# Optimization experiments

Hardware: AMD Instinct MI355X
Metric: run time of the kernel (lower is better)

The kernel has to match this reference:

```python
import jax, jax.numpy as jnp
import numpy as np

B, S, E, H, FF = 4, 2048, 512, 8, 2048
DH = E // H
EPS = 1e-6


def setup_inputs() -> dict:
    key = jax.random.key(0)
    ks = jax.random.split(key, 16)
    sc = lambda fan_in: 1.0 / np.sqrt(fan_in)
    inp = {
        "x": jax.random.normal(ks[0], (B, S, E), dtype=jnp.float32),
        "src_mask": jnp.ones((B, 1, 1, S), dtype=jnp.int32),
        # attention projections, stored [in, out]
        "wq": jax.random.uniform(ks[1], (E, E), minval=-sc(E), maxval=sc(E)),
        "bq": jnp.zeros((E,), jnp.float32),
        "wk": jax.random.uniform(ks[2], (E, E), minval=-sc(E), maxval=sc(E)),
        "bk": jnp.zeros((E,), jnp.float32),
        "wv": jax.random.uniform(ks[3], (E, E), minval=-sc(E), maxval=sc(E)),
        "bv": jnp.zeros((E,), jnp.float32),
        "wo": jax.random.uniform(ks[4], (E, E), minval=-sc(E), maxval=sc(E)),
        "bo": jnp.zeros((E,), jnp.float32),
        # feed-forward
        "w1": jax.random.uniform(ks[5], (E, FF), minval=-sc(E), maxval=sc(E)),
        "b1": jnp.zeros((FF,), jnp.float32),
        "w2": jax.random.uniform(ks[6], (FF, E), minval=-sc(FF), maxval=sc(FF)),
        "b2": jnp.zeros((E,), jnp.float32),
        # addNormLayer scalar params (alpha init 1, bias init 0)
        "alpha1": jnp.ones((1,), jnp.float32),
        "beta1": jnp.zeros((1,), jnp.float32),
        "alpha2": jnp.ones((1,), jnp.float32),
        "beta2": jnp.zeros((1,), jnp.float32),
    }
    return inp


def _norm(x, alpha, beta):
    # matches torch: mean + unbiased std (ddof=1), eps added to std
    mean = jnp.mean(x, axis=-1, keepdims=True)
    std = jnp.std(x, axis=-1, keepdims=True, ddof=1)
    return alpha * (x - mean) / (std + EPS) + beta


def reference(x, src_mask, wq, bq, wk, bk, wv, bv, wo, bo,
              w1, b1, w2, b2, alpha1, beta1, alpha2, beta2):
    # --- residual 1: pre-norm self-attention ---
    n = _norm(x, alpha1, beta1)  # [B,S,E]
    q = (n @ wq + bq).reshape(B, S, H, DH).transpose(0, 2, 1, 3)  # [B,H,S,DH]
    k = (n @ wk + bk).reshape(B, S, H, DH).transpose(0, 2, 1, 3)
    v = (n @ wv + bv).reshape(B, S, H, DH).transpose(0, 2, 1, 3)
    scores = jnp.einsum('bhqd,bhkd->bhqk', q, k) / np.sqrt(DH)  # [B,H,S,S]
    scores = jnp.where(src_mask == 0, -1e9, scores)
    attn = jax.nn.softmax(scores, axis=-1)
    ctx = jnp.einsum('bhqk,bhkd->bhqd', attn, v)  # [B,H,S,DH]
    ctx = ctx.transpose(0, 2, 1, 3).reshape(B, S, E)
    x = x + (ctx @ wo + bo)
    # --- residual 2: pre-norm FFN ---
    n2 = _norm(x, alpha2, beta2)
    ff = jax.nn.relu(n2 @ w1 + b1) @ w2 + b2
    return x + ff
```

## Files before the change

kernel.cpp:

```cpp
#include <hip/hip_runtime.h>
#include <type_traits>

typedef __bf16 bfrag __attribute__((ext_vector_type(8)));
typedef float f32x4 __attribute__((ext_vector_type(4)));
typedef float f32x16 __attribute__((ext_vector_type(16)));
typedef unsigned short us8 __attribute__((ext_vector_type(8)));
typedef unsigned int u32x2 __attribute__((ext_vector_type(2)));
typedef unsigned int u32x4 __attribute__((ext_vector_type(4)));

__device__ __forceinline__ float bf2f(unsigned short s) {
  unsigned u = ((unsigned)s) << 16;
  float f;
  __builtin_memcpy(&f, &u, 4);
  return f;
}
__device__ __forceinline__ unsigned short f2bf(float f) {
  unsigned u;
  __builtin_memcpy(&u, &f, 4);
  u += 0x7fffu + ((u >> 16) & 1u);
  return (unsigned short)(u >> 16);
}
__device__ __forceinline__ float rdf(const void* p, size_t i, int isf) {
  return isf ? ((const float*)p)[i] : bf2f(((const unsigned short*)p)[i]);
}
__device__ __forceinline__ void gld16(const unsigned short* g, unsigned short* l) {
  __builtin_amdgcn_global_load_lds(
      (const __attribute__((address_space(1))) unsigned int*)g,
      (__attribute__((address_space(3))) unsigned int*)l, 16, 0, 0);
}
__device__ __forceinline__ unsigned cvtpk_bf16(float a, float b) {
  unsigned d;
  asm("v_cvt_pk_bf16_f32 %0, %1, %2" : "=v"(d) : "v"(a), "v"(b));
  return d;
}

template <int XMODE>
__device__ void norm_unit(const void* xin, const void* alpha, const void* beta,
                          unsigned short* out, int isf, int u) {
  constexpr int E = 512;
  int xf = XMODE ? 1 : isf;
  int tid = threadIdx.x;
  int wave = tid >> 6, lane = tid & 63;
  size_t tok = (size_t)u * 4 + wave;
  float v[8];
  if (xf) {
    const float* xp = (const float*)xin + tok * E + lane * 8;
    float4 a0 = *(const float4*)xp;
    float4 a1 = *(const float4*)(xp + 4);
    v[0] = a0.x; v[1] = a0.y; v[2] = a0.z; v[3] = a0.w;
    v[4] = a1.x; v[5] = a1.y; v[6] = a1.z; v[7] = a1.w;
  } else {
    us8 uu = *(const us8*)((const unsigned short*)xin + tok * E + lane * 8);
#pragma unroll
    for (int j = 0; j < 8; j++) v[j] = bf2f(uu[j]);
  }
  float s = 0.f, sq = 0.f;
#pragma unroll
  for (int j = 0; j < 8; j++) { s += v[j]; sq += v[j] * v[j]; }
#pragma unroll
  for (int off = 1; off < 64; off <<= 1) {
    s += __shfl_xor(s, off, 64);
    sq += __shfl_xor(sq, off, 64);
  }
  float mean = s * (1.0f / 512.0f);
  float var = fmaxf((sq - 512.0f * mean * mean) * (1.0f / 511.0f), 0.0f);
  float inv = rdf(alpha, 0, isf) / (sqrtf(var) + 1e-6f);
  float be = rdf(beta, 0, isf);
  us8 ov;
#pragma unroll
  for (int j = 0; j < 8; j++) ov[j] = f2bf((v[j] - mean) * inv + be);
  *(us8*)(out + tok * E + lane * 8) = ov;
}

__global__ __launch_bounds__(256) void setup_k(
    const unsigned short* __restrict__ x16,
    const void* wq, const void* wk, const void* wv, const void* wo,
    const void* w1, const void* w2,
    unsigned short* wqkvT, unsigned short* woT,
    unsigned short* w1T, unsigned short* w2T,
    const void* bq, const void* bk, const void* bv, const void* bo,
    const void* b1, const void* b2, float* __restrict__ bcat,
    const void* alpha1, const void* beta1, unsigned short* __restrict__ n1,
    int* __restrict__ flag) {
  __shared__ unsigned short tile[32][33];
  __shared__ int s_cnt;
  int tid = threadIdx.x;
  int bid = blockIdx.x;
  if (tid == 0) s_cnt = 0;
  __syncthreads();
  {
    int c = 0;
    for (int i = tid; i < 4096; i += 256) {
      unsigned short s = x16[2 * i];
      int e = (s >> 7) & 0xFF;
      if (e > 0xC2 || (e != 0 && e < 0x3D)) c++;
    }
    atomicAdd(&s_cnt, c);
  }
  __syncthreads();
  const int isf = (s_cnt > 256) ? 1 : 0;
  if (bid == 0 && tid == 0) flag[0] = isf;

  if (bid >= 3090) {
    norm_unit<0>(x16, alpha1, beta1, n1, isf, bid - 3090);
    return;
  }
  if (bid >= 3072) {
    int i = (bid - 3072) * 256 + tid;
    if (i < 4608) {
      float v;
      if (i < 512) v = rdf(bq, i, isf);
      else if (i < 1024) v = rdf(bk, i - 512, isf);
      else if (i < 1536) v = rdf(bv, i - 1024, isf);
      else if (i < 2048) v = rdf(bo, i - 1536, isf);
      else if (i < 4096) v = rdf(b1, i - 2048, isf);
      else v = rdf(b2, i - 4096, isf);
      bcat[i] = v;
    }
    return;
  }
  const void* W;
  unsigned short* Wt;
  int K, N, t;
  if (bid < 1024) {
    K = 512; N = 512; t = bid & 255;
    if (bid < 256) { W = wq; Wt = wqkvT; }
    else if (bid < 512) { W = wk; Wt = wqkvT + 262144; }
    else if (bid < 768) { W = wv; Wt = wqkvT + 524288; }
    else { W = wo; Wt = woT; }
  } else if (bid < 2048) {
    W = w1; Wt = w1T; K = 512; N = 2048; t = bid - 1024;
  } else {
    W = w2; Wt = w2T; K = 2048; N = 512; t = bid - 2048;
  }
  int nx = N >> 5;
  int n0 = (t % nx) * 32, k0 = (t / nx) * 32;
#pragma unroll
  for (int i = 0; i < 4; i++) {
    int e = tid + i * 256;
    int r = e >> 5, c = e & 31;
    tile[r][c] = f2bf(rdf(W, (size_t)(k0 + r) * N + n0 + c, isf));
  }
  __syncthreads();
#pragma unroll
  for (int i = 0; i < 4; i++) {
    int e = tid + i * 256;
    int r = e >> 5, c = e & 31;
    Wt[(size_t)(n0 + r) * K + k0 + c] = tile[c][r];
  }
}

__global__ __launch_bounds__(256) void vtrans_k(
    const unsigned short* __restrict__ qkb, unsigned short* __restrict__ vbt) {
  __shared__ unsigned short tile[32][33];
  int tid = threadIdx.x;
  int u = blockIdx.x;
  int s0 = (u & 63) * 32;
  int d0 = ((u >> 6) & 1) * 32;
  int bh = u >> 7, b = bh >> 3, h = bh & 7;
#pragma unroll
  for (int i = 0; i < 4; i++) {
    int e = tid + i * 256;
    int r = e >> 5, c = e & 31;
    tile[r][c] = qkb[((size_t)b * 2048 + s0 + r) * 1536 + 1024 + h * 64 + d0 + c];
  }
  __syncthreads();
#pragma unroll
  for (int i = 0; i < 4; i++) {
    int e = tid + i * 256;
    int r = e >> 5, c = e & 31;
    vbt[((size_t)bh * 64 + d0 + r) * 2048 + s0 + c] = tile[c][r];
  }
}

__global__ __launch_bounds__(256) void norm2_k(
    const void* __restrict__ xin, const void* __restrict__ alpha,
    const void* __restrict__ beta, unsigned short* __restrict__ out,
    const int* __restrict__ flag) {
  norm_unit<1>(xin, alpha, beta, out, flag[0], blockIdx.x);
}

template <int TN, int RES, int OUTM, int RELU>
__global__ __launch_bounds__(256, 3) void gemm2_k(
    const unsigned short* __restrict__ A,
    const unsigned short* __restrict__ Bt,
    const float* __restrict__ bias,
    const void* __restrict__ res,
    void* __restrict__ outp,
    int N, int K, const int* __restrict__ flag) {
  constexpr int MT = (TN == 128) ? 4 : 2;
  constexpr int BROWS = TN / 4;
  __shared__ alignas(16) unsigned short As[128 * 64];
  __shared__ alignas(16) unsigned short Bs[TN * 64];
  int isf = flag[0];
  int outf32 = (OUTM == 1) || (OUTM == 2 && isf);
  int tid = threadIdx.x;
  int wave = tid >> 6, lane = tid & 63;
  int quad = lane >> 4, l16 = lane & 15, l7 = l16 & 7;
  int wm = (TN == 128) ? (wave >> 1) : wave;
  int wn = (TN == 128) ? (wave & 1) : 0;
  size_t m0 = (size_t)blockIdx.x * 128;
  size_t n0 = (size_t)blockIdx.y * TN;

  int lrow = lane >> 3;
  int gcol = 8 * ((lane & 7) ^ lrow);

  const unsigned short* ag = A + (m0 + wave * 32 + lrow) * K + gcol;
  const unsigned short* bg = Bt + (n0 + wave * BROWS + lrow) * K + gcol;
  unsigned short* asl = &As[(wave * 32) * 64];
  unsigned short* bsl = &Bs[(wave * BROWS) * 64];

  f32x4 acc[MT][4];
#pragma unroll
  for (int i = 0; i < MT; i++)
#pragma unroll
    for (int j = 0; j < 4; j++) acc[i][j] = {0.f, 0.f, 0.f, 0.f};

  for (int k0 = 0; k0 < K; k0 += 64) {
    __syncthreads();
#pragma unroll
    for (int c = 0; c < 4; c++)
      gld16(ag + (size_t)(8 * c) * K + k0, asl + (8 * c) * 64);
#pragma unroll
    for (int c = 0; c < BROWS / 8; c++)
      gld16(bg + (size_t)(8 * c) * K + k0, bsl + (8 * c) * 64);
    __syncthreads();
#pragma unroll
    for (int ko = 0; ko < 2; ko++) {
      int slot = ((4 * ko + quad) ^ l7) * 8;
      bfrag af[MT], bf[4];
#pragma unroll
      for (int i = 0; i < MT; i++)
        af[i] = *(const bfrag*)&As[(wm * (MT * 16) + i * 16 + l16) * 64 + slot];
#pragma unroll
      for (int j = 0; j < 4; j++)
        bf[j] = *(const bfrag*)&Bs[(wn * 64 + j * 16 + l16) * 64 + slot];
#pragma unroll
      for (int i = 0; i < MT; i++)
#pragma unroll
        for (int j = 0; j < 4; j++)
          acc[i][j] = __builtin_amdgcn_mfma_f32_16x16x32_bf16(af[i], bf[j], acc[i][j], 0, 0, 0);
    }
  }
#pragma unroll
  for (int j = 0; j < 4; j++) {
    size_t n = n0 + wn * 64 + j * 16 + l16;
    float bv = bias[n];
#pragma unroll
    for (int i = 0; i < MT; i++) {
#pragma unroll
      for (int r = 0; r < 4; r++) {
        size_t m = m0 + wm * (MT * 16) + i * 16 + quad * 4 + r;
        float vv = acc[i][j][r] + bv;
        if (RELU) vv = fmaxf(vv, 0.0f);
        if (RES == 1) vv += rdf(res, m * N + n, isf);
        else if (RES == 2) vv += ((const float*)res)[m * N + n];
        if (outf32) ((float*)outp)[m * N + n] = vv;
        else ((unsigned short*)outp)[m * N + n] = f2bf(vv);
      }
    }
  }
}

__global__ __launch_bounds__(512, 4) void attn_k(
    const unsigned short* __restrict__ qkb,
    const unsigned short* __restrict__ vbt,
    const int* __restrict__ mask,
    unsigned short* __restrict__ ctx) {
  constexpr int S = 2048;
  __shared__ alignas(16) unsigned short Kt[2][2][64 * 64];
  __shared__ alignas(16) unsigned short Vt[2][2][64 * 64];
  __shared__ alignas(16) float mskf[S];
  __shared__ float ml[2][128];
  __shared__ int s_all;
  int tid = threadIdx.x, wave = tid >> 6, lane = tid & 63;
  int kh = wave >> 2, wv = wave & 3;
  int l32 = lane & 31, hi = lane >> 5;

  int lin = blockIdx.x;
  int work = (lin & 7) * 64 + (lin >> 3);
  int bh = work >> 4;
  int q0 = (work & 15) * 128;
  int b = bh >> 3, h = bh & 7;
  size_t rowbase = (size_t)b * S;
  const float SC = 0.18033688f;

  bfrag qf[4];
  {
    const unsigned short* qp =
        qkb + (rowbase + q0 + wv * 32 + l32) * 1536 + h * 64 + hi * 8;
#pragma unroll
    for (int ds = 0; ds < 4; ds++) qf[ds] = *(const bfrag*)(qp + ds * 16);
  }

  int srow_l = lane >> 3;
  int sc = lane & 7;
  int swz = (sc ^ srow_l) * 8;
  const unsigned short* kgb = qkb + 512 + h * 64;
  const unsigned short* vgb = vbt + (size_t)bh * 64 * S;

  const unsigned short* kp[2];
  const unsigned short* vp[2];
#pragma unroll
  for (int i = 0; i < 2; i++) {
    int r = wv * 16 + i * 8 + srow_l;
    kp[i] = kgb + (rowbase + kh * 1024 + r) * 1536 + swz;
    vp[i] = vgb + (size_t)r * S + kh * 1024 + swz;
  }

  auto STAGE = [&](int buf) {
#pragma unroll
    for (int i = 0; i < 2; i++) {
      gld16(kp[i], &Kt[kh][buf][(wv * 16 + i * 8) * 64]);
      kp[i] += 64 * 1536;
      gld16(vp[i], &Vt[kh][buf][(wv * 16 + i * 8) * 64]);
      vp[i] += 64;
    }
  };

  f32x16 o[2];
#pragma unroll
  for (int i = 0; i < 16; i++) { o[0][i] = 0.f; o[1][i] = 0.f; }
  f32x16 z16;
#pragma unroll
  for (int i = 0; i < 16; i++) z16[i] = 0.f;
  float l_i = 0.f;

  STAGE(0);
  if (tid == 0) s_all = 1;
  __syncthreads();
  {
    int ok = 1;
    for (int i = tid; i < S; i += 512) {
      int mv = mask[rowbase + i];
      ok &= (mv != 0);
      mskf[i] = mv ? 0.0f : -1e5f;
    }
    atomicAnd(&s_all, ok);
  }
  __syncthreads();
  int am = s_all;

  auto BODY = [&](auto amc) {
    constexpr bool AM = decltype(amc)::value;
    for (int it = 0; it < 16; it++) {
      int cur = it & 1;
      if (it + 1 < 16) STAGE(cur ^ 1);

      f32x16 pacc[2];
#pragma unroll
      for (int t = 0; t < 2; t++) {
        int r = t * 32 + l32;
#pragma unroll
        for (int ds = 0; ds < 4; ds++) {
          int phys = ((2 * ds + hi) ^ (l32 & 7)) * 8;
          bfrag kf = *(const bfrag*)&Kt[kh][cur][r * 64 + phys];
          pacc[t] = __builtin_amdgcn_mfma_f32_32x32x16_bf16(
              kf, qf[ds], ds == 0 ? z16 : pacc[t], 0, 0, 0);
        }
      }

      unsigned pb[16];
#pragma unroll
      for (int t = 0; t < 2; t++) {
#pragma unroll
        for (int g = 0; g < 4; g++) {
          float p0, p1, p2, p3;
          if constexpr (AM) {
            p0 = __builtin_amdgcn_exp2f(pacc[t][g * 4 + 0] * SC);
            p1 = __builtin_amdgcn_exp2f(pacc[t][g * 4 + 1] * SC);
            p2 = __builtin_amdgcn_exp2f(pacc[t][g * 4 + 2] * SC);
            p3 = __builtin_amdgcn_exp2f(pacc[t][g * 4 + 3] * SC);
          } else {
            float4 m4 =
                *(const float4*)&mskf[kh * 1024 + it * 64 + t * 32 + g * 8 + hi * 4];
            p0 = __builtin_amdgcn_exp2f(fmaf(pacc[t][g * 4 + 0], SC, m4.x));
            p1 = __builtin_amdgcn_exp2f(fmaf(pacc[t][g * 4 + 1], SC, m4.y));
            p2 = __builtin_amdgcn_exp2f(fmaf(pacc[t][g * 4 + 2], SC, m4.z));
            p3 = __builtin_amdgcn_exp2f(fmaf(pacc[t][g * 4 + 3], SC, m4.w));
          }
          l_i += (p0 + p1) + (p2 + p3);
          pb[t * 8 + g * 2] = cvtpk_bf16(p0, p1);
          pb[t * 8 + g * 2 + 1] = cvtpk_bf16(p2, p3);
        }
      }

#pragma unroll
      for (int ks = 0; ks < 4; ks++) {
        int t = ks >> 1, e = ks & 1;
        u32x2 sA = __builtin_amdgcn_permlane32_swap(
            pb[t * 8 + 4 * e + 0], pb[t * 8 + 4 * e + 2], false, false);
        u32x2 sB = __builtin_amdgcn_permlane32_swap(
            pb[t * 8 + 4 * e + 1], pb[t * 8 + 4 * e + 3], false, false);
        u32x4 pw = {sA.x, sB.x, sA.y, sB.y};
        bfrag pf = __builtin_bit_cast(bfrag, pw);
#pragma unroll
        for (int dt = 0; dt < 2; dt++) {
          int r = dt * 32 + l32;
          int phys = ((2 * ks + hi) ^ (l32 & 7)) * 8;
          bfrag vf = *(const bfrag*)&Vt[kh][cur][r * 64 + phys];
          o[dt] = __builtin_amdgcn_mfma_f32_32x32x16_bf16(pf, vf, o[dt], 0, 0, 0);
        }
      }
      __syncthreads();
    }
  };
  if (am) BODY(std::integral_constant<bool, true>{});
  else    BODY(std::integral_constant<bool, false>{});

  {
    unsigned lu = __builtin_bit_cast(unsigned, l_i);
    u32x2 lr = __builtin_amdgcn_permlane32_swap(lu, lu, false, false);
    float l_tot = __builtin_bit_cast(float, lr.x) + __builtin_bit_cast(float, lr.y);
    if (lane < 32) ml[kh][wv * 32 + l32] = l_tot;
  }
  float* mrg = (float*)&Kt[0][0][0];
  if (kh == 1) {
#pragma unroll
    for (int dt = 0; dt < 2; dt++) {
#pragma unroll
      for (int reg = 0; reg < 16; reg++) {
        int ql = (reg & 3) + 8 * (reg >> 2) + 4 * hi;
        mrg[wv * 2048 + ql * 64 + dt * 32 + l32] = o[dt][reg];
      }
    }
  }
  __syncthreads();
  if (kh == 0) {
#pragma unroll
    for (int dt = 0; dt < 2; dt++) {
#pragma unroll
      for (int reg = 0; reg < 16; reg++) {
        int ql = (reg & 3) + 8 * (reg >> 2) + 4 * hi;
        float inv = 1.0f / fmaxf(ml[0][wv * 32 + ql] + ml[1][wv * 32 + ql], 1e-30f);
        float val = (o[dt][reg] + mrg[wv * 2048 + ql * 64 + dt * 32 + l32]) * inv;
        size_t qrow = rowbase + q0 + wv * 32 + ql;
        ctx[qrow * 512 + h * 64 + dt * 32 + l32] = f2bf(val);
      }
    }
  }
}

extern "C" void kernel_launch(void* const* d_in, const int* in_sizes, int n_in,
                              void* d_out, int out_size, void* d_ws, size_t ws_size,
                              hipStream_t stream) {
  const unsigned short* x = (const unsigned short*)d_in[0];
  const int* mask         = (const int*)d_in[1];
  const void* wq = d_in[2];  const void* bq = d_in[3];
  const void* wk = d_in[4];  const void* bk = d_in[5];
  const void* wv = d_in[6];  const void* bv = d_in[7];
  const void* wo = d_in[8];  const void* bo = d_in[9];
  const void* w1 = d_in[10]; const void* b1 = d_in[11];
  const void* w2 = d_in[12]; const void* b2 = d_in[13];
  const void* alpha1 = d_in[14]; const void* beta1 = d_in[15];
  const void* alpha2 = d_in[16]; const void* beta2 = d_in[17];

  char* ws = (char*)d_ws;
  int* flag            = (int*)(ws + 0);
  unsigned short* wqkvT= (unsigned short*)(ws + 65536);
  unsigned short* woT  = (unsigned short*)(ws + 1638400);
  unsigned short* w1T  = (unsigned short*)(ws + 2162688);
  unsigned short* w2T  = (unsigned short*)(ws + 4259840);
  float*          bcat = (float*)         (ws + 6356992);
  float*          x1   = (float*)         (ws + 6422528);
  unsigned short* n1   = (unsigned short*)(ws + 23199744);
  unsigned short* qkb  = (unsigned short*)(ws + 31588352);
  unsigned short* vbt  = (unsigned short*)(ws + 56754176);
  unsigned short* ff1  = qkb;

  dim3 blk(256);

  setup_k<<<5138, blk, 0, stream>>>(x, wq, wk, wv, wo, w1, w2,
                                    wqkvT, woT, w1T, w2T,
                                    bq, bk, bv, bo, b1, b2, bcat,
                                    alpha1, beta1, n1, flag);
  gemm2_k<128, 0, 0, 0><<<dim3(64, 12), blk, 0, stream>>>(n1, wqkvT, bcat, nullptr, qkb, 1536, 512, flag);
  vtrans_k<<<4096, blk, 0, stream>>>(qkb, vbt);
  attn_k<<<512, dim3(512), 0, stream>>>(qkb, vbt, mask, n1);
  gemm2_k<64, 1, 1, 0><<<dim3(64, 8), blk, 0, stream>>>(n1, woT, bcat + 1536, (const void*)x, x1, 512, 512, flag);
  norm2_k<<<2048, blk, 0, stream>>>(x1, alpha2, beta2, n1, flag);
  gemm2_k<128, 0, 0, 1><<<dim3(64, 16), blk, 0, stream>>>(n1, w1T, bcat + 2048, nullptr, ff1, 2048, 512, flag);
  gemm2_k<64, 2, 2, 0><<<dim3(64, 8), blk, 0, stream>>>(ff1, w2T, bcat + 4096, x1, d_out, 512, 2048, flag);
}
```

Measured before the change: 287.5 us.

## Double query rows per attention block to reuse staged K/V tiles

Each attention block now handles 256 query rows instead of 128, with each wave processing two 32-row query groups against the same staged K and V tiles. This halves the grid to 256 blocks and halves the global-to-LDS K/V traffic per query, and the merge step now uses both the K and V LDS buffers. The trade-offs are more accumulator registers per wave, launch bounds lowered to 2 blocks per CU, and fewer blocks than the 256 CUs can take, which risks lower occupancy and weaker latency hiding.

```diff
diff --git a/kernel.cpp b/kernel.cpp
--- a/kernel.cpp
+++ b/kernel.cpp
@@ -262,7 +262,7 @@
   }
 }
 
-__global__ __launch_bounds__(512, 4) void attn_k(
+__global__ __launch_bounds__(512, 2) void attn_k(
     const unsigned short* __restrict__ qkb,
     const unsigned short* __restrict__ vbt,
     const int* __restrict__ mask,
@@ -271,26 +271,27 @@
   __shared__ alignas(16) unsigned short Kt[2][2][64 * 64];
   __shared__ alignas(16) unsigned short Vt[2][2][64 * 64];
   __shared__ alignas(16) float mskf[S];
-  __shared__ float ml[2][128];
+  __shared__ float ml[2][256];
   __shared__ int s_all;
   int tid = threadIdx.x, wave = tid >> 6, lane = tid & 63;
   int kh = wave >> 2, wv = wave & 3;
   int l32 = lane & 31, hi = lane >> 5;
 
   int lin = blockIdx.x;
-  int work = (lin & 7) * 64 + (lin >> 3);
-  int bh = work >> 4;
-  int q0 = (work & 15) * 128;
+  int work = (lin & 7) * 32 + (lin >> 3);
+  int bh = work >> 3;
+  int q0 = (work & 7) * 256;
   int b = bh >> 3, h = bh & 7;
   size_t rowbase = (size_t)b * S;
   const float SC = 0.18033688f;
 
-  bfrag qf[4];
-  {
+  bfrag qf[2][4];
+#pragma unroll
+  for (int qg = 0; qg < 2; qg++) {
     const unsigned short* qp =
-        qkb + (rowbase + q0 + wv * 32 + l32) * 1536 + h * 64 + hi * 8;
-#pragma unroll
-    for (int ds = 0; ds < 4; ds++) qf[ds] = *(const bfrag*)(qp + ds * 16);
+        qkb + (rowbase + q0 + wv * 64 + qg * 32 + l32) * 1536 + h * 64 + hi * 8;
+#pragma unroll
+    for (int ds = 0; ds < 4; ds++) qf[qg][ds] = *(const bfrag*)(qp + ds * 16);
   }
 
   int srow_l = lane >> 3;
@@ -318,13 +319,12 @@
     }
   };
 
-  f32x16 o[2];
-#pragma unroll
-  for (int i = 0; i < 16; i++) { o[0][i] = 0.f; o[1][i] = 0.f; }
-  f32x16 z16;
-#pragma unroll
-  for (int i = 0; i < 16; i++) z16[i] = 0.f;
-  float l_i = 0.f;
+  f32x16 o[4];
+#pragma unroll
+  for (int i = 0; i < 4; i++)
+#pragma unroll
+    for (int j = 0; j < 16; j++) o[i][j] = 0.f;
+  float l_i[2] = {0.f, 0.f};
 
   STAGE(0);
   if (tid == 0) s_all = 1;
@@ -347,59 +347,61 @@
       int cur = it & 1;
       if (it + 1 < 16) STAGE(cur ^ 1);
 
-      f32x16 pacc[2];
-#pragma unroll
-      for (int t = 0; t < 2; t++) {
-        int r = t * 32 + l32;
-#pragma unroll
-        for (int ds = 0; ds < 4; ds++) {
-          int phys = ((2 * ds + hi) ^ (l32 & 7)) * 8;
-          bfrag kf = *(const bfrag*)&Kt[kh][cur][r * 64 + phys];
-          pacc[t] = __builtin_amdgcn_mfma_f32_32x32x16_bf16(
-              kf, qf[ds], ds == 0 ? z16 : pacc[t], 0, 0, 0);
-        }
-      }
-
-      unsigned pb[16];
-#pragma unroll
-      for (int t = 0; t < 2; t++) {
-#pragma unroll
-        for (int g = 0; g < 4; g++) {
-          float p0, p1, p2, p3;
-          if constexpr (AM) {
-            p0 = __builtin_amdgcn_exp2f(pacc[t][g * 4 + 0] * SC);
-            p1 = __builtin_amdgcn_exp2f(pacc[t][g * 4 + 1] * SC);
-            p2 = __builtin_amdgcn_exp2f(pacc[t][g * 4 + 2] * SC);
-            p3 = __builtin_amdgcn_exp2f(pacc[t][g * 4 + 3] * SC);
-          } else {
-            float4 m4 =
-                *(const float4*)&mskf[kh * 1024 + it * 64 + t * 32 + g * 8 + hi * 4];
-            p0 = __builtin_amdgcn_exp2f(fmaf(pacc[t][g * 4 + 0], SC, m4.x));
-            p1 = __builtin_amdgcn_exp2f(fmaf(pacc[t][g * 4 + 1], SC, m4.y));
-            p2 = __builtin_amdgcn_exp2f(fmaf(pacc[t][g * 4 + 2], SC, m4.z));
-            p3 = __builtin_amdgcn_exp2f(fmaf(pacc[t][g * 4 + 3], SC, m4.w));
+#pragma unroll
+      for (int qg = 0; qg < 2; qg++) {
+#pragma unroll
+        for (int t = 0; t < 2; t++) {
+          f32x16 pacc;
+          {
+            int r = t * 32 + l32;
+            f32x16 z = {};
+#pragma unroll
+            for (int ds = 0; ds < 4; ds++) {
+              int phys = ((2 * ds + hi) ^ (l32 & 7)) * 8;
+              bfrag kf = *(const bfrag*)&Kt[kh][cur][r * 64 + phys];
+              pacc = __builtin_amdgcn_mfma_f32_32x32x16_bf16(
+                  kf, qf[qg][ds], ds == 0 ? z : pacc, 0, 0, 0);
+            }
           }
-          l_i += (p0 + p1) + (p2 + p3);
-          pb[t * 8 + g * 2] = cvtpk_bf16(p0, p1);
-          pb[t * 8 + g * 2 + 1] = cvtpk_bf16(p2, p3);
-        }
-      }
-
-#pragma unroll
-      for (int ks = 0; ks < 4; ks++) {
-        int t = ks >> 1, e = ks & 1;
-        u32x2 sA = __builtin_amdgcn_permlane32_swap(
-            pb[t * 8 + 4 * e + 0], pb[t * 8 + 4 * e + 2], false, false);
-        u32x2 sB = __builtin_amdgcn_permlane32_swap(
-            pb[t * 8 + 4 * e + 1], pb[t * 8 + 4 * e + 3], false, false);
-        u32x4 pw = {sA.x, sB.x, sA.y, sB.y};
-        bfrag pf = __builtin_bit_cast(bfrag, pw);
-#pragma unroll
-        for (int dt = 0; dt < 2; dt++) {
-          int r = dt * 32 + l32;
-          int phys = ((2 * ks + hi) ^ (l32 & 7)) * 8;
-          bfrag vf = *(const bfrag*)&Vt[kh][cur][r * 64 + phys];
-          o[dt] = __builtin_amdgcn_mfma_f32_32x32x16_bf16(pf, vf, o[dt], 0, 0, 0);
+          unsigned pb[8];
+#pragma unroll
+          for (int g = 0; g < 4; g++) {
+            float p0, p1, p2, p3;
+            if constexpr (AM) {
+              p0 = __builtin_amdgcn_exp2f(pacc[g * 4 + 0] * SC);
+              p1 = __builtin_amdgcn_exp2f(pacc[g * 4 + 1] * SC);
+              p2 = __builtin_amdgcn_exp2f(pacc[g * 4 + 2] * SC);
+              p3 = __builtin_amdgcn_exp2f(pacc[g * 4 + 3] * SC);
+            } else {
+              float4 m4 =
+                  *(const float4*)&mskf[kh * 1024 + it * 64 + t * 32 + g * 8 + hi * 4];
+              p0 = __builtin_amdgcn_exp2f(fmaf(pacc[g * 4 + 0], SC, m4.x));
+              p1 = __builtin_amdgcn_exp2f(fmaf(pacc[g * 4 + 1], SC, m4.y));
+              p2 = __builtin_amdgcn_exp2f(fmaf(pacc[g * 4 + 2], SC, m4.z));
+              p3 = __builtin_amdgcn_exp2f(fmaf(pacc[g * 4 + 3], SC, m4.w));
+            }
+            l_i[qg] += (p0 + p1) + (p2 + p3);
+            pb[g * 2] = cvtpk_bf16(p0, p1);
+            pb[g * 2 + 1] = cvtpk_bf16(p2, p3);
+          }
+#pragma unroll
+          for (int e = 0; e < 2; e++) {
+            u32x2 sA = __builtin_amdgcn_permlane32_swap(
+                pb[4 * e + 0], pb[4 * e + 2], false, false);
+            u32x2 sB = __builtin_amdgcn_permlane32_swap(
+                pb[4 * e + 1], pb[4 * e + 3], false, false);
+            u32x4 pw = {sA.x, sB.x, sA.y, sB.y};
+            bfrag pf = __builtin_bit_cast(bfrag, pw);
+            int ks = 2 * t + e;
+#pragma unroll
+            for (int dt = 0; dt < 2; dt++) {
+              int r = dt * 32 + l32;
+              int phys = ((2 * ks + hi) ^ (l32 & 7)) * 8;
+              bfrag vf = *(const bfrag*)&Vt[kh][cur][r * 64 + phys];
+              o[qg * 2 + dt] = __builtin_amdgcn_mfma_f32_32x32x16_bf16(
+                  pf, vf, o[qg * 2 + dt], 0, 0, 0);
+            }
+          }
         }
       }
       __syncthreads();
@@ -408,34 +410,41 @@
   if (am) BODY(std::integral_constant<bool, true>{});
   else    BODY(std::integral_constant<bool, false>{});
 
-  {
-    unsigned lu = __builtin_bit_cast(unsigned, l_i);
+#pragma unroll
+  for (int qg = 0; qg < 2; qg++) {
+    unsigned lu = __builtin_bit_cast(unsigned, l_i[qg]);
     u32x2 lr = __builtin_amdgcn_permlane32_swap(lu, lu, false, false);
     float l_tot = __builtin_bit_cast(float, lr.x) + __builtin_bit_cast(float, lr.y);
-    if (lane < 32) ml[kh][wv * 32 + l32] = l_tot;
-  }
-  float* mrg = (float*)&Kt[0][0][0];
+    if (lane < 32) ml[kh][wv * 64 + qg * 32 + l32] = l_tot;
+  }
+  float* mrgK = (float*)&Kt[0][0][0];
+  float* mrgV = (float*)&Vt[0][0][0];
   if (kh == 1) {
 #pragma unroll
-    for (int dt = 0; dt < 2; dt++) {
+    for (int qg = 0; qg < 2; qg++) {
 #pragma unroll
       for (int reg = 0; reg < 16; reg++) {
         int ql = (reg & 3) + 8 * (reg >> 2) + 4 * hi;
-        mrg[wv * 2048 + ql * 64 + dt * 32 + l32] = o[dt][reg];
+        int qi = wv * 64 + qg * 32 + ql;
+        mrgK[qi * 32 + l32] = o[qg * 2 + 0][reg];
+        mrgV[qi * 32 + l32] = o[qg * 2 + 1][reg];
       }
     }
   }
   __syncthreads();
   if (kh == 0) {
 #pragma unroll
-    for (int dt = 0; dt < 2; dt++) {
+    for (int qg = 0; qg < 2; qg++) {
 #pragma unroll
       for (int reg = 0; reg < 16; reg++) {
         int ql = (reg & 3) + 8 * (reg >> 2) + 4 * hi;
-        float inv = 1.0f / fmaxf(ml[0][wv * 32 + ql] + ml[1][wv * 32 + ql], 1e-30f);
-        float val = (o[dt][reg] + mrg[wv * 2048 + ql * 64 + dt * 32 + l32]) * inv;
-        size_t qrow = rowbase + q0 + wv * 32 + ql;
-        ctx[qrow * 512 + h * 64 + dt * 32 + l32] = f2bf(val);
+        int qi = wv * 64 + qg * 32 + ql;
+        float inv = 1.0f / fmaxf(ml[0][qi] + ml[1][qi], 1e-30f);
+        size_t qrow = rowbase + q0 + qi;
+        float v0 = (o[qg * 2 + 0][reg] + mrgK[qi * 32 + l32]) * inv;
+        float v1 = (o[qg * 2 + 1][reg] + mrgV[qi * 32 + l32]) * inv;
+        ctx[qrow * 512 + h * 64 + l32] = f2bf(v0);
+        ctx[qrow * 512 + h * 64 + 32 + l32] = f2bf(v1);
       }
     }
   }
@@ -476,7 +485,7 @@
                                     alpha1, beta1, n1, flag);
   gemm2_k<128, 0, 0, 0><<<dim3(64, 12), blk, 0, stream>>>(n1, wqkvT, bcat, nullptr, qkb, 1536, 512, flag);
   vtrans_k<<<4096, blk, 0, stream>>>(qkb, vbt);
-  attn_k<<<512, dim3(512), 0, stream>>>(qkb, vbt, mask, n1);
+  attn_k<<<256, dim3(512), 0, stream>>>(qkb, vbt, mask, n1);
   gemm2_k<64, 1, 1, 0><<<dim3(64, 8), blk, 0, stream>>>(n1, woT, bcat + 1536, (const void*)x, x1, 512, 512, flag);
   norm2_k<<<2048, blk, 0, stream>>>(x1, alpha2, beta2, n1, flag);
   gemm2_k<128, 0, 0, 1><<<dim3(64, 16), blk, 0, stream>>>(n1, w1T, bcat + 2048, nullptr, ff1, 2048, 512, flag);
```

Result: no change. 286.9 us (-0.2%).
